# Optimization experiments

Measured on AMD Instinct MI355X. Metric: run time of the kernel, lower is better.

The kernel has to match this reference:

```python
import jax, jax.numpy as jnp
import numpy as np
import math

NHEADS = 16
CAUSAL = True
NEG_INF = -1e18


def setup_inputs() -> dict:
    key = jax.random.key(0)
    kq, kk, kv = jax.random.split(key, 3)
    B, S, D = 4, 8192, 1024
    q = jax.random.normal(kq, (B, S, D), dtype=jnp.float32)
    k = jax.random.normal(kk, (B, S, D), dtype=jnp.float32)
    v = jax.random.normal(kv, (B, S, D), dtype=jnp.float32)
    return {"q": q, "k": k, "v": v}


def reference(q, k, v):
    # Faithful to the torch code: it views (B,S,H*hd)->(B,S,H,hd) WITHOUT
    # transposing heads to dim 1, so matmul(q, k^T) is an (H,H) score matrix
    # per token -- attention across HEADS, causal mask/softmax over heads.
    B, S, D = q.shape
    hd = D // NHEADS
    qh = q.reshape(B, S, NHEADS, hd)
    kh = k.reshape(B, S, NHEADS, hd)
    vh = v.reshape(B, S, NHEADS, hd)
    # scores: (B, S, H, H)
    scores = jnp.einsum('bsqd,bskd->bsqk', qh, kh) / math.sqrt(hd)
    if CAUSAL:
        mask = jnp.tril(jnp.ones((NHEADS, NHEADS), dtype=bool))
        scores = jnp.where(mask, scores, jnp.asarray(NEG_INF, scores.dtype))
    attn = jax.nn.softmax(scores, axis=-1)
    out = jnp.einsum('bsqk,bskd->bsqd', attn, vh)
    return out.reshape(B, S, D)
```

## Files before the change

kernel.cpp:

```cpp
#include <hip/hip_runtime.h>
#include <math.h>

#define NHEADS 16
#define HD 64
#define DMODEL 1024
#define QK_PAD 68

__global__ __launch_bounds__(256) void temporal_attn_kernel(
    const float* __restrict__ q,
    const float* __restrict__ k,
    const float* __restrict__ v,
    float* __restrict__ out)
{
    __shared__ float  qs[NHEADS * QK_PAD];
    __shared__ float  ks[NHEADS * QK_PAD];
    __shared__ float4 vs[NHEADS * (HD / 4)];
    __shared__ float  ps[NHEADS][NHEADS + 1];

    const int t = threadIdx.x;
    const size_t base = (size_t)blockIdx.x * DMODEL;
    const int r = t >> 4;
    const int c = t & 15;

    const float4 qv = ((const float4*)(q + base))[t];
    const float4 kv = ((const float4*)(k + base))[t];
    const float4 vv = ((const float4*)(v + base))[t];
    *((float4*)&qs[r * QK_PAD + 4 * c]) = qv;
    *((float4*)&ks[r * QK_PAD + 4 * c]) = kv;
    vs[t] = vv;
    __syncthreads();

    const float4* qi = (const float4*)&qs[r * QK_PAD];
    const float4* kj = (const float4*)&ks[c * QK_PAD];
    float acc = 0.f;
    #pragma unroll
    for (int d = 0; d < HD / 4; ++d) {
        const float4 a = qi[d];
        const float4 b = kj[d];
        acc = fmaf(a.x, b.x, acc);
        acc = fmaf(a.y, b.y, acc);
        acc = fmaf(a.z, b.z, acc);
        acc = fmaf(a.w, b.w, acc);
    }
    acc *= 0.125f;
    if (c > r) acc = -1e30f;

    float m = acc;
    #pragma unroll
    for (int mask = 8; mask >= 1; mask >>= 1)
        m = fmaxf(m, __shfl_xor(m, mask, 16));
    const float p = __expf(acc - m);
    float s = p;
    #pragma unroll
    for (int mask = 8; mask >= 1; mask >>= 1)
        s += __shfl_xor(s, mask, 16);
    ps[r][c] = p / s;
    __syncthreads();

    float4 o = make_float4(0.f, 0.f, 0.f, 0.f);
    #pragma unroll
    for (int j = 0; j < NHEADS; ++j) {
        const float  pij = ps[r][j];
        const float4 vj  = vs[j * (HD / 4) + c];
        o.x = fmaf(pij, vj.x, o.x);
        o.y = fmaf(pij, vj.y, o.y);
        o.z = fmaf(pij, vj.z, o.z);
        o.w = fmaf(pij, vj.w, o.w);
    }
    ((float4*)(out + base))[t] = o;
}

extern "C" void kernel_launch(void* const* d_in, const int* in_sizes, int n_in,
                              void* d_out, int out_size, void* d_ws, size_t ws_size,
                              hipStream_t stream) {
    const float* q = (const float*)d_in[0];
    const float* k = (const float*)d_in[1];
    const float* v = (const float*)d_in[2];
    float* o = (float*)d_out;
    const int ntok = in_sizes[0] / DMODEL;
    temporal_attn_kernel<<<ntok, 256, 0, stream>>>(q, k, v, o);
}
```

Baseline: 96.78 us.

## Process one token per wavefront with fp16 QK dot products and register tiling

Each 64-lane wavefront now handles a whole token, four tokens per block, so the block-wide __syncthreads barriers are gone and each wave works on its own shared-memory slice. Q and K are converted to fp16 and the score matrix is computed with packed half2 FMAs in 2x2 register tiles. PV uses 4-row register tiling. The kernel is memory bound, so the compute savings may matter little. The fp16 scores reduce accuracy, and the code has no intra-wave barrier between LDS writes and reads, relying on lockstep wave execution.

Result: slower. 100.9 us (+4.3%).

```diff
diff --git a/kernel.cpp b/kernel.cpp
--- a/kernel.cpp
+++ b/kernel.cpp
@@ -1,10 +1,25 @@
 #include <hip/hip_runtime.h>
+#include <hip/hip_fp16.h>
 #include <math.h>
 
 #define NHEADS 16
 #define HD 64
 #define DMODEL 1024
-#define QK_PAD 68
+#define TOKW 4
+
+#define TOKF 2560
+
+union F4H {
+    float4  f;
+    __half2 h[4];
+};
+
+__device__ __forceinline__ void fma4(float4& o, float p, const float4& v) {
+    o.x = fmaf(p, v.x, o.x);
+    o.y = fmaf(p, v.y, o.y);
+    o.z = fmaf(p, v.z, o.z);
+    o.w = fmaf(p, v.w, o.w);
+}
 
 __global__ __launch_bounds__(256) void temporal_attn_kernel(
     const float* __restrict__ q,
@@ -12,62 +27,124 @@
     const float* __restrict__ v,
     float* __restrict__ out)
 {
-    __shared__ float  qs[NHEADS * QK_PAD];
-    __shared__ float  ks[NHEADS * QK_PAD];
-    __shared__ float4 vs[NHEADS * (HD / 4)];
-    __shared__ float  ps[NHEADS][NHEADS + 1];
+    __shared__ float smem[TOKW * TOKF];
 
-    const int t = threadIdx.x;
-    const size_t base = (size_t)blockIdx.x * DMODEL;
-    const int r = t >> 4;
-    const int c = t & 15;
+    const int wave = threadIdx.x >> 6;
+    const int lane = threadIdx.x & 63;
+    const size_t base = ((size_t)blockIdx.x * TOKW + wave) * DMODEL;
 
-    const float4 qv = ((const float4*)(q + base))[t];
-    const float4 kv = ((const float4*)(k + base))[t];
-    const float4 vv = ((const float4*)(v + base))[t];
-    *((float4*)&qs[r * QK_PAD + 4 * c]) = qv;
-    *((float4*)&ks[r * QK_PAD + 4 * c]) = kv;
-    vs[t] = vv;
-    __syncthreads();
+    float* qs = smem + wave * TOKF;
+    float* ks = qs + 576;
+    float* vs = qs + 1152;
+    float* ps = qs + 2240;
 
-    const float4* qi = (const float4*)&qs[r * QK_PAD];
-    const float4* kj = (const float4*)&ks[c * QK_PAD];
-    float acc = 0.f;
-    #pragma unroll
-    for (int d = 0; d < HD / 4; ++d) {
-        const float4 a = qi[d];
-        const float4 b = kj[d];
-        acc = fmaf(a.x, b.x, acc);
-        acc = fmaf(a.y, b.y, acc);
-        acc = fmaf(a.z, b.z, acc);
-        acc = fmaf(a.w, b.w, acc);
+    const int si = lane >> 2;
+    const int sc = lane & 3;
+    const float4* qg = (const float4*)(q + base);
+    const float4* kg = (const float4*)(k + base);
+    const float4* vg = (const float4*)(v + base);
+    float4 ql[4], kl[4], vl[4];
+#pragma unroll
+    for (int j = 0; j < 4; ++j) ql[j] = qg[4 * lane + j];
+#pragma unroll
+    for (int j = 0; j < 4; ++j) kl[j] = kg[4 * lane + j];
+#pragma unroll
+    for (int j = 0; j < 4; ++j) vl[j] = vg[4 * lane + j];
+
+    F4H qh[2], kh[2];
+#pragma unroll
+    for (int j = 0; j < 2; ++j) {
+        qh[j].h[0] = __floats2half2_rn(ql[2*j].x,   ql[2*j].y);
+        qh[j].h[1] = __floats2half2_rn(ql[2*j].z,   ql[2*j].w);
+        qh[j].h[2] = __floats2half2_rn(ql[2*j+1].x, ql[2*j+1].y);
+        qh[j].h[3] = __floats2half2_rn(ql[2*j+1].z, ql[2*j+1].w);
+        kh[j].h[0] = __floats2half2_rn(kl[2*j].x,   kl[2*j].y);
+        kh[j].h[1] = __floats2half2_rn(kl[2*j].z,   kl[2*j].w);
+        kh[j].h[2] = __floats2half2_rn(kl[2*j+1].x, kl[2*j+1].y);
+        kh[j].h[3] = __floats2half2_rn(kl[2*j+1].z, kl[2*j+1].w);
     }
-    acc *= 0.125f;
-    if (c > r) acc = -1e30f;
+    *(float4*)&qs[36 * si + 8 * sc + 0] = qh[0].f;
+    *(float4*)&qs[36 * si + 8 * sc + 4] = qh[1].f;
+    *(float4*)&ks[36 * si + 8 * sc + 0] = kh[0].f;
+    *(float4*)&ks[36 * si + 8 * sc + 4] = kh[1].f;
+#pragma unroll
+    for (int j = 0; j < 4; ++j)
+        *(float4*)&vs[68 * si + 16 * sc + 4 * j] = vl[j];
 
-    float m = acc;
-    #pragma unroll
-    for (int mask = 8; mask >= 1; mask >>= 1)
-        m = fmaxf(m, __shfl_xor(m, mask, 16));
-    const float p = __expf(acc - m);
-    float s = p;
-    #pragma unroll
-    for (int mask = 8; mask >= 1; mask >>= 1)
-        s += __shfl_xor(s, mask, 16);
-    ps[r][c] = p / s;
-    __syncthreads();
+    const int ri = lane >> 3;
+    const int ci = lane & 7;
+    const __half2 z2 = __float2half2_rn(0.f);
+    __half2 a00 = z2, a01 = z2, a10 = z2, a11 = z2;
+#pragma unroll
+    for (int d = 0; d < 8; ++d) {
+        F4H qa, qb, ka, kb;
+        qa.f = *(const float4*)&qs[36 * (2 * ri)     + 4 * d];
+        qb.f = *(const float4*)&qs[36 * (2 * ri + 1) + 4 * d];
+        ka.f = *(const float4*)&ks[36 * (2 * ci)     + 4 * d];
+        kb.f = *(const float4*)&ks[36 * (2 * ci + 1) + 4 * d];
+#pragma unroll
+        for (int m = 0; m < 4; ++m) {
+            a00 = __hfma2(qa.h[m], ka.h[m], a00);
+            a01 = __hfma2(qa.h[m], kb.h[m], a01);
+            a10 = __hfma2(qb.h[m], ka.h[m], a10);
+            a11 = __hfma2(qb.h[m], kb.h[m], a11);
+        }
+    }
+    float s00 = (__low2float(a00) + __high2float(a00)) * 0.125f;
+    float s01 = (__low2float(a01) + __high2float(a01)) * 0.125f;
+    float s10 = (__low2float(a10) + __high2float(a10)) * 0.125f;
+    float s11 = (__low2float(a11) + __high2float(a11)) * 0.125f;
+    {
+        const int r0 = 2 * ri, r1 = 2 * ri + 1, c0 = 2 * ci, c1 = 2 * ci + 1;
+        if (c0 > r0) s00 = -1e30f;
+        if (c1 > r0) s01 = -1e30f;
+        if (c0 > r1) s10 = -1e30f;
+        if (c1 > r1) s11 = -1e30f;
+    }
+#pragma unroll
+    for (int a = 0; a < 2; ++a) {
+        float x0 = a ? s10 : s00;
+        float x1 = a ? s11 : s01;
+        float m = fmaxf(x0, x1);
+        m = fmaxf(m, __shfl_xor(m, 1));
+        m = fmaxf(m, __shfl_xor(m, 2));
+        m = fmaxf(m, __shfl_xor(m, 4));
+        float e0 = __expf(x0 - m);
+        float e1 = __expf(x1 - m);
+        float sum = e0 + e1;
+        sum += __shfl_xor(sum, 1);
+        sum += __shfl_xor(sum, 2);
+        sum += __shfl_xor(sum, 4);
+        const float inv = 1.0f / sum;
+        float2 pw = make_float2(e0 * inv, e1 * inv);
+        *(float2*)&ps[20 * (2 * ri + a) + 2 * ci] = pw;
+    }
 
-    float4 o = make_float4(0.f, 0.f, 0.f, 0.f);
-    #pragma unroll
-    for (int j = 0; j < NHEADS; ++j) {
-        const float  pij = ps[r][j];
-        const float4 vj  = vs[j * (HD / 4) + c];
-        o.x = fmaf(pij, vj.x, o.x);
-        o.y = fmaf(pij, vj.y, o.y);
-        o.z = fmaf(pij, vj.z, o.z);
-        o.w = fmaf(pij, vj.w, o.w);
+    const int r4 = lane >> 4;
+    const int c4 = lane & 15;
+    float4 o0 = make_float4(0.f, 0.f, 0.f, 0.f);
+    float4 o1 = o0, o2 = o0, o3 = o0;
+#pragma unroll
+    for (int jb = 0; jb < 4; ++jb) {
+        const float4 p0 = *(const float4*)&ps[20 * (0 + r4)  + 4 * jb];
+        const float4 p1 = *(const float4*)&ps[20 * (4 + r4)  + 4 * jb];
+        const float4 p2 = *(const float4*)&ps[20 * (8 + r4)  + 4 * jb];
+        const float4 p3 = *(const float4*)&ps[20 * (12 + r4) + 4 * jb];
+        float4 vj;
+        vj = *(const float4*)&vs[68 * (4 * jb + 0) + 4 * c4];
+        fma4(o0, p0.x, vj); fma4(o1, p1.x, vj); fma4(o2, p2.x, vj); fma4(o3, p3.x, vj);
+        vj = *(const float4*)&vs[68 * (4 * jb + 1) + 4 * c4];
+        fma4(o0, p0.y, vj); fma4(o1, p1.y, vj); fma4(o2, p2.y, vj); fma4(o3, p3.y, vj);
+        vj = *(const float4*)&vs[68 * (4 * jb + 2) + 4 * c4];
+        fma4(o0, p0.z, vj); fma4(o1, p1.z, vj); fma4(o2, p2.z, vj); fma4(o3, p3.z, vj);
+        vj = *(const float4*)&vs[68 * (4 * jb + 3) + 4 * c4];
+        fma4(o0, p0.w, vj); fma4(o1, p1.w, vj); fma4(o2, p2.w, vj); fma4(o3, p3.w, vj);
     }
-    ((float4*)(out + base))[t] = o;
+    float4* og = (float4*)(out + base);
+    og[0 * 64 + lane] = o0;
+    og[1 * 64 + lane] = o1;
+    og[2 * 64 + lane] = o2;
+    og[3 * 64 + lane] = o3;
 }
 
 extern "C" void kernel_launch(void* const* d_in, const int* in_sizes, int n_in,
@@ -78,5 +155,6 @@
     const float* v = (const float*)d_in[2];
     float* o = (float*)d_out;
     const int ntok = in_sizes[0] / DMODEL;
-    temporal_attn_kernel<<<ntok, 256, 0, stream>>>(q, k, v, o);
+    const int nblk = ntok / TOKW;
+    temporal_attn_kernel<<<nblk, 256, 0, stream>>>(q, k, v, o);
 }
```
